# Kernel optimization log

Hardware: AMD Instinct MI355X
Metric: run time of the kernel (lower is better)

## Reference

```python
import jax, jax.numpy as jnp
import numpy as np

S = 3136        # tokens (56x56 patch grid, single image segment -> full attention)
H = 16          # num_heads
D = 80          # head_dim (= head_dim_ori = PADDING_HEAD_DIM)
HID = H * D     # 1280
SCALE = 1.0 / float(np.sqrt(D))  # qkScale = 1/sqrt(head_dim_ori)


def _rope_tables(s, d, base=10000.0):
    # rotate_half style: cos/sin of shape [s, d], duplicated over the two halves
    half = d // 2
    inv_freq = 1.0 / (base ** (np.arange(0, half, dtype=np.float32) / half))
    freqs = np.outer(np.arange(s, dtype=np.float32), inv_freq)  # [s, d/2]
    emb = np.concatenate([freqs, freqs], axis=-1)               # [s, d]
    return jnp.asarray(np.cos(emb)), jnp.asarray(np.sin(emb))


def setup_inputs() -> dict:
    key = jax.random.key(0)
    ks = jax.random.split(key, 6)
    cos, sin = _rope_tables(S, D)
    return {
        "hidden_states": jax.random.normal(ks[0], (S, HID), jnp.float32),
        "x_norm": jax.random.normal(ks[1], (S, HID), jnp.float32),
        "qkv_w": jax.random.normal(ks[2], (3 * HID, HID), jnp.float32) * 0.02,
        "qkv_b": jax.random.normal(ks[3], (3 * HID,), jnp.float32) * 0.02,
        "proj_w": jax.random.normal(ks[4], (HID, HID), jnp.float32) * 0.02,
        "proj_b": jax.random.normal(ks[5], (HID,), jnp.float32) * 0.02,
        "cos": cos,
        "sin": sin,
    }


def _rotate_half(x):
    x1, x2 = jnp.split(x, 2, axis=-1)
    return jnp.concatenate([-x2, x1], axis=-1)


def reference(hidden_states, x_norm, qkv_w, qkv_b, proj_w, proj_b, cos, sin):
    # fused QKV linear (transposeB=True) + split into q,k,v along last dim
    qkv = x_norm @ qkv_w.T + qkv_b                      # [S, 3*HID]
    q, k, v = jnp.split(qkv, 3, axis=-1)                # each [S, HID]
    q = q.reshape(S, H, D)
    k = k.reshape(S, H, D)
    v = v.reshape(S, H, D)
    # inline RoPE on q and k (rotate_half over full head_dim)
    c = cos[:, None, :]; s = sin[:, None, :]           # [S,1,D]
    q = q * c + _rotate_half(q) * s
    k = k * c + _rotate_half(k) * s
    # full self-attention (PA_ENCODER, single segment = seq_len S)
    scores = jnp.einsum('shd,thd->hst', q, k) * SCALE   # [H,S,S]
    probs = jax.nn.softmax(scores, axis=-1)
    attn = jnp.einsum('hst,thd->shd', probs, v)         # [S,H,D]
    attn = attn.reshape(S, HID)
    # output projection + residual add
    out = attn @ proj_w.T + proj_b
    return hidden_states + out
```

## Files before the change

kernel.cpp:

```cpp
#include <hip/hip_runtime.h>
#include <hip/hip_bf16.h>

#define S_   3136
#define H_   16
#define D_   80
#define DP_  96
#define HID_ 1280

typedef short  bf16x8 __attribute__((ext_vector_type(8)));
typedef short  bf16x4 __attribute__((ext_vector_type(4)));
typedef float  f32x4  __attribute__((ext_vector_type(4)));

__device__ __forceinline__ float b2f(unsigned short u) {
    union { unsigned int i; float f; } c;
    c.i = ((unsigned int)u) << 16;
    return c.f;
}
__device__ __forceinline__ unsigned short f2b(float f) {
    union { unsigned int i; float f; } c;
    c.f = f;
    unsigned int x = c.i;
    unsigned int lsb = (x >> 16) & 1u;
    x += 0x7fffu + lsb;
    return (unsigned short)(x >> 16);
}

#define N4_X 1003520
#define N4_Q 1228800
#define N4_P 409600

__global__ __launch_bounds__(256)
void cast3_kernel(const float* __restrict__ x0, unsigned short* __restrict__ y0,
                  const float* __restrict__ x1, unsigned short* __restrict__ y1,
                  const float* __restrict__ x2, unsigned short* __restrict__ y2)
{
    int i = blockIdx.x * 256 + threadIdx.x;
    const float* src; unsigned short* dst;
    if (i < N4_X)               { src = x0; dst = y0; }
    else if (i < N4_X + N4_Q)   { src = x1; dst = y1; i -= N4_X; }
    else if (i < N4_X + N4_Q + N4_P) { src = x2; dst = y2; i -= N4_X + N4_Q; }
    else return;
    float4 v = ((const float4*)src)[i];
    ushort4 o;
    o.x = f2b(v.x); o.y = f2b(v.y); o.z = f2b(v.z); o.w = f2b(v.w);
    ((ushort4*)dst)[i] = o;
}

#define ASTR 40

__global__ __launch_bounds__(256)
void qkv_mfma_kernel(const unsigned short* __restrict__ Ab,
                     const unsigned short* __restrict__ Wb,
                     const float* __restrict__ bias,
                     unsigned short* __restrict__ qo, unsigned short* __restrict__ ko,
                     unsigned short* __restrict__ vtb)
{
    __shared__ __align__(16) short As[128][ASTR];
    __shared__ __align__(16) short Bs[128][ASTR];
    int m0 = blockIdx.x * 128;
    int n0 = blockIdx.y * 128;
    int t = threadIdx.x;
    int wave = t >> 6, lane = t & 63, lq = lane & 15, quad = lane >> 4;
    int wr = wave >> 1, wc = wave & 1;

    int r0  = t >> 2;
    int r1  = r0 + 64;
    int kc0 = (t & 3) << 3;
    const unsigned short* pa0 = Ab + (size_t)min(m0 + r0, S_ - 1) * HID_ + kc0;
    const unsigned short* pa1 = Ab + (size_t)min(m0 + r1, S_ - 1) * HID_ + kc0;
    const unsigned short* pb0 = Wb + (size_t)(n0 + r0) * HID_ + kc0;
    const unsigned short* pb1 = Wb + (size_t)(n0 + r1) * HID_ + kc0;
    short* sa0 = &As[r0][kc0];
    short* sa1 = &As[r1][kc0];
    short* sb0 = &Bs[r0][kc0];
    short* sb1 = &Bs[r1][kc0];

    const bf16x8* afp[4]; const bf16x8* bfp[4];
    #pragma unroll
    for (int i = 0; i < 4; ++i) {
        afp[i] = (const bf16x8*)&As[wr * 64 + i * 16 + lq][quad * 8];
        bfp[i] = (const bf16x8*)&Bs[wc * 64 + i * 16 + lq][quad * 8];
    }

    f32x4 acc[4][4];
    #pragma unroll
    for (int i = 0; i < 4; ++i)
        #pragma unroll
        for (int j = 0; j < 4; ++j) acc[i][j] = (f32x4){0.f, 0.f, 0.f, 0.f};

    bf16x8 va0 = *(const bf16x8*)(pa0);
    bf16x8 va1 = *(const bf16x8*)(pa1);
    bf16x8 vb0 = *(const bf16x8*)(pb0);
    bf16x8 vb1 = *(const bf16x8*)(pb1);

    for (int kt = 0; kt < HID_; kt += 32) {
        __syncthreads();
        *(bf16x8*)sa0 = va0; *(bf16x8*)sa1 = va1;
        *(bf16x8*)sb0 = vb0; *(bf16x8*)sb1 = vb1;
        __syncthreads();
        if (kt + 32 < HID_) {
            va0 = *(const bf16x8*)(pa0 + kt + 32);
            va1 = *(const bf16x8*)(pa1 + kt + 32);
            vb0 = *(const bf16x8*)(pb0 + kt + 32);
            vb1 = *(const bf16x8*)(pb1 + kt + 32);
        }
        bf16x8 af[4], bfr[4];
        #pragma unroll
        for (int i = 0; i < 4; ++i) af[i]  = *afp[i];
        #pragma unroll
        for (int j = 0; j < 4; ++j) bfr[j] = *bfp[j];
        #pragma unroll
        for (int i = 0; i < 4; ++i)
            #pragma unroll
            for (int j = 0; j < 4; ++j)
                acc[i][j] = __builtin_amdgcn_mfma_f32_16x16x32_bf16(af[i], bfr[j], acc[i][j], 0, 0, 0);
    }

    #pragma unroll
    for (int i = 0; i < 4; ++i)
        #pragma unroll
        for (int j = 0; j < 4; ++j)
            #pragma unroll
            for (int reg = 0; reg < 4; ++reg) {
                int row = m0 + wr * 64 + i * 16 + quad * 4 + reg;
                if (row >= S_) continue;
                int col = n0 + wc * 64 + j * 16 + lq;
                float val = acc[i][j][reg] + bias[col];
                int which = col / HID_;
                int rem   = col - which * HID_;
                int h     = rem / D_;
                int d     = rem - h * D_;
                if (which == 0)      qo[((size_t)h * S_ + row) * D_ + d] = f2b(val);
                else if (which == 1) ko[((size_t)h * S_ + row) * D_ + d] = f2b(val);
                else                 vtb[((size_t)h * D_ + d) * S_ + row] = f2b(val);
            }
}

__global__ __launch_bounds__(256)
void proj_mfma_kernel(const unsigned short* __restrict__ Ab,
                      const unsigned short* __restrict__ Wb,
                      const float* __restrict__ bias, const float* __restrict__ hidden,
                      float* __restrict__ out)
{
    __shared__ __align__(16) short As[64][ASTR];
    __shared__ __align__(16) short Bs[64][ASTR];
    int m0 = blockIdx.x * 64;
    int n0 = blockIdx.y * 64;
    int t = threadIdx.x;
    int wave = t >> 6, lane = t & 63, lq = lane & 15, quad = lane >> 4;
    int wr = wave >> 1, wc = wave & 1;

    int r  = t >> 2;
    int kc0 = (t & 3) << 3;
    const unsigned short* pa = Ab + (size_t)(m0 + r) * HID_ + kc0;
    const unsigned short* pb = Wb + (size_t)(n0 + r) * HID_ + kc0;
    short* sa = &As[r][kc0];
    short* sb = &Bs[r][kc0];

    const bf16x8* afp[2]; const bf16x8* bfp[2];
    #pragma unroll
    for (int i = 0; i < 2; ++i) {
        afp[i] = (const bf16x8*)&As[wr * 32 + i * 16 + lq][quad * 8];
        bfp[i] = (const bf16x8*)&Bs[wc * 32 + i * 16 + lq][quad * 8];
    }

    f32x4 acc[2][2];
    #pragma unroll
    for (int i = 0; i < 2; ++i)
        #pragma unroll
        for (int j = 0; j < 2; ++j) acc[i][j] = (f32x4){0.f, 0.f, 0.f, 0.f};

    bf16x8 va = *(const bf16x8*)(pa);
    bf16x8 vb = *(const bf16x8*)(pb);

    for (int kt = 0; kt < HID_; kt += 32) {
        __syncthreads();
        *(bf16x8*)sa = va;
        *(bf16x8*)sb = vb;
        __syncthreads();
        if (kt + 32 < HID_) {
            va = *(const bf16x8*)(pa + kt + 32);
            vb = *(const bf16x8*)(pb + kt + 32);
        }
        bf16x8 af[2], bfr[2];
        #pragma unroll
        for (int i = 0; i < 2; ++i) af[i]  = *afp[i];
        #pragma unroll
        for (int j = 0; j < 2; ++j) bfr[j] = *bfp[j];
        #pragma unroll
        for (int i = 0; i < 2; ++i)
            #pragma unroll
            for (int j = 0; j < 2; ++j)
                acc[i][j] = __builtin_amdgcn_mfma_f32_16x16x32_bf16(af[i], bfr[j], acc[i][j], 0, 0, 0);
    }

    #pragma unroll
    for (int i = 0; i < 2; ++i)
        #pragma unroll
        for (int j = 0; j < 2; ++j)
            #pragma unroll
            for (int reg = 0; reg < 4; ++reg) {
                int row = m0 + wr * 32 + i * 16 + quad * 4 + reg;
                int col = n0 + wc * 32 + j * 16 + lq;
                out[(size_t)row * HID_ + col] =
                    acc[i][j][reg] + bias[col] + hidden[(size_t)row * HID_ + col];
            }
}

__global__ void rope_kernel(const unsigned short* __restrict__ q, const unsigned short* __restrict__ k,
                            const float* __restrict__ cost, const float* __restrict__ sint,
                            unsigned short* __restrict__ qb, unsigned short* __restrict__ kb)
{
    const float QSCALE = 0.11180339887498949f * 1.4426950408889634f;
    int idx = blockIdx.x * 256 + threadIdx.x;
    const int total = H_ * S_ * 40;
    if (idx >= total) return;
    int d  = idx % 40;
    int hs = idx / 40;
    int s  = hs % S_;
    size_t base  = (size_t)hs * D_;
    size_t base9 = (size_t)hs * DP_;
    float c1 = cost[s * D_ + d];
    float s1 = sint[s * D_ + d];
    float c2 = cost[s * D_ + d + 40];
    float s2 = sint[s * D_ + d + 40];
    float x1 = b2f(q[base + d]), x2 = b2f(q[base + d + 40]);
    qb[base9 + d]      = f2b((x1 * c1 - x2 * s1) * QSCALE);
    qb[base9 + d + 40] = f2b((x2 * c2 + x1 * s2) * QSCALE);
    x1 = b2f(k[base + d]); x2 = b2f(k[base + d + 40]);
    kb[base9 + d]      = f2b(x1 * c1 - x2 * s1);
    kb[base9 + d + 40] = f2b(x2 * c2 + x1 * s2);
    if (d < 16) {
        qb[base9 + 80 + d] = 0;
        kb[base9 + 80 + d] = 0;
    }
}

#define KSTRIDE 104
#define VSTRIDE 72
#define PSTRIDE 68

__global__ __launch_bounds__(256)
void attn_kernel(const unsigned short* __restrict__ Qb,
                 const unsigned short* __restrict__ Kb,
                 const unsigned short* __restrict__ Vtb,
                 unsigned short* __restrict__ attnb)
{
    __shared__ __align__(16) short Ks[64][KSTRIDE];
    __shared__ __align__(16) short Vs[2][96][VSTRIDE];
    __shared__ __align__(16) short Ps[4][16][PSTRIDE];

    int h   = blockIdx.y;
    int qb0 = blockIdx.x * 64;
    int t    = threadIdx.x;
    int wave = t >> 6;
    int lane = t & 63;
    int lq   = lane & 15;
    int quad = lane >> 4;

    const unsigned short* Qrow = Qb + ((size_t)h * S_ + qb0 + wave * 16 + lq) * DP_;
    bf16x8 qf[3];
    #pragma unroll
    for (int kc = 0; kc < 3; ++kc)
        qf[kc] = *(const bf16x8*)(Qrow + kc * 32 + quad * 8);

    f32x4 O[5];
    #pragma unroll
    for (int dt = 0; dt < 5; ++dt) O[dt] = (f32x4){0.f, 0.f, 0.f, 0.f};
    float l_acc[4] = {0.f, 0.f, 0.f, 0.f};

    int srow = t & 63;
    int w    = t >> 6;
    int vr0  = t >> 3;
    int vc   = (t & 7) << 3;
    const unsigned short* Kg = Kb  + (size_t)h * S_ * DP_ + (size_t)srow * DP_;
    const unsigned short* Vg = Vtb + (size_t)h * D_ * S_;
    short* kl0 = &Ks[srow][(w    ) * 8];
    short* kl1 = &Ks[srow][(w + 4) * 8];
    short* kl2 = &Ks[srow][(w + 8) * 8];

    const int NKB = S_ / 64;
    bf16x8 pk0, pk1, pk2, pv0, pv1, pv2;
    {
        pk0 = *(const bf16x8*)(Kg + (w    ) * 8);
        pk1 = *(const bf16x8*)(Kg + (w + 4) * 8);
        pk2 = *(const bf16x8*)(Kg + (w + 8) * 8);
        const unsigned short* vg = Vg + vc;
        pv0 = *(const bf16x8*)(vg + (size_t)(vr0     ) * S_);
        pv1 = *(const bf16x8*)(vg + (size_t)(vr0 + 32) * S_);
        pv2 = *(const bf16x8*)(vg + (size_t)(vr0 + 64) * S_);
    }

    for (int kb = 0; kb < NKB; ++kb) {
        int vb = kb & 1;
        __syncthreads();
        *(bf16x8*)kl0 = pk0;
        *(bf16x8*)kl1 = pk1;
        *(bf16x8*)kl2 = pk2;
        *(bf16x8*)&Vs[vb][vr0     ][vc] = pv0;
        *(bf16x8*)&Vs[vb][vr0 + 32][vc] = pv1;
        *(bf16x8*)&Vs[vb][vr0 + 64][vc] = pv2;
        __syncthreads();

        if (kb + 1 < NKB) {
            const unsigned short* kg = Kg + (size_t)(kb + 1) * 64 * DP_;
            pk0 = *(const bf16x8*)(kg + (w    ) * 8);
            pk1 = *(const bf16x8*)(kg + (w + 4) * 8);
            pk2 = *(const bf16x8*)(kg + (w + 8) * 8);
            const unsigned short* vg = Vg + (kb + 1) * 64 + vc;
            pv0 = *(const bf16x8*)(vg + (size_t)(vr0     ) * S_);
            pv1 = *(const bf16x8*)(vg + (size_t)(vr0 + 32) * S_);
            pv2 = *(const bf16x8*)(vg + (size_t)(vr0 + 64) * S_);
        }

        f32x4 sc[4];
        #pragma unroll
        for (int nt = 0; nt < 4; ++nt) {
            sc[nt] = (f32x4){0.f, 0.f, 0.f, 0.f};
            #pragma unroll
            for (int kc = 0; kc < 3; ++kc) {
                bf16x8 kf = *(const bf16x8*)&Ks[nt * 16 + lq][kc * 32 + quad * 8];
                sc[nt] = __builtin_amdgcn_mfma_f32_16x16x32_bf16(qf[kc], kf, sc[nt], 0, 0, 0);
            }
        }

        if (kb > 0) {
            const short (*Vp)[VSTRIDE] = Vs[vb ^ 1];
            #pragma unroll
            for (int kc = 0; kc < 2; ++kc) {
                union { bf16x8 v8; bf16x4 v4[2]; } pf;
                pf.v4[0] = *(const bf16x4*)&Ps[wave][lq][kc * 32 + quad * 8];
                pf.v4[1] = *(const bf16x4*)&Ps[wave][lq][kc * 32 + quad * 8 + 4];
                #pragma unroll
                for (int dt = 0; dt < 5; ++dt) {
                    bf16x8 vf = *(const bf16x8*)&Vp[dt * 16 + lq][kc * 32 + quad * 8];
                    O[dt] = __builtin_amdgcn_mfma_f32_16x16x32_bf16(pf.v8, vf, O[dt], 0, 0, 0);
                }
            }
        }

        #pragma unroll
        for (int reg = 0; reg < 4; ++reg) {
            float p0 = exp2f(sc[0][reg]);
            float p1 = exp2f(sc[1][reg]);
            float p2 = exp2f(sc[2][reg]);
            float p3 = exp2f(sc[3][reg]);
            l_acc[reg] += (p0 + p1) + (p2 + p3);
            int prow = quad * 4 + reg;
            Ps[wave][prow][ 0 + lq] = (short)(__float_as_uint(p0) >> 16);
            Ps[wave][prow][16 + lq] = (short)(__float_as_uint(p1) >> 16);
            Ps[wave][prow][32 + lq] = (short)(__float_as_uint(p2) >> 16);
            Ps[wave][prow][48 + lq] = (short)(__float_as_uint(p3) >> 16);
        }
    }

    {
        const short (*Vp)[VSTRIDE] = Vs[(NKB - 1) & 1];
        #pragma unroll
        for (int kc = 0; kc < 2; ++kc) {
            union { bf16x8 v8; bf16x4 v4[2]; } pf;
            pf.v4[0] = *(const bf16x4*)&Ps[wave][lq][kc * 32 + quad * 8];
            pf.v4[1] = *(const bf16x4*)&Ps[wave][lq][kc * 32 + quad * 8 + 4];
            #pragma unroll
            for (int dt = 0; dt < 5; ++dt) {
                bf16x8 vf = *(const bf16x8*)&Vp[dt * 16 + lq][kc * 32 + quad * 8];
                O[dt] = __builtin_amdgcn_mfma_f32_16x16x32_bf16(pf.v8, vf, O[dt], 0, 0, 0);
            }
        }
    }

    #pragma unroll
    for (int reg = 0; reg < 4; ++reg) {
        float l = l_acc[reg];
        #pragma unroll
        for (int off = 1; off < 16; off <<= 1)
            l += __shfl_xor(l, off, 16);
        float linv = 1.0f / l;
        int s = qb0 + wave * 16 + quad * 4 + reg;
        unsigned short* orow = attnb + (size_t)s * HID_ + h * D_;
        #pragma unroll
        for (int dt = 0; dt < 5; ++dt)
            orow[dt * 16 + lq] = f2b(O[dt][reg] * linv);
    }
}

extern "C" void kernel_launch(void* const* d_in, const int* in_sizes, int n_in,
                              void* d_out, int out_size, void* d_ws, size_t ws_size,
                              hipStream_t stream)
{
    const float* hidden = (const float*)d_in[0];
    const float* x_norm = (const float*)d_in[1];
    const float* qkv_w  = (const float*)d_in[2];
    const float* qkv_b  = (const float*)d_in[3];
    const float* proj_w = (const float*)d_in[4];
    const float* proj_b = (const float*)d_in[5];
    const float* cost   = (const float*)d_in[6];
    const float* sint   = (const float*)d_in[7];
    float* out = (float*)d_out;

    unsigned short* w      = (unsigned short*)d_ws;
    unsigned short* qbuf   = w;
    unsigned short* kbuf   = qbuf + 4014080;
    unsigned short* vtb    = kbuf + 4014080;
    unsigned short* kbb    = vtb + 4064256;
    unsigned short* xb     = kbb + 4816896;
    unsigned short* wqkvb  = xb + 4014080;
    unsigned short* wprojb = wqkvb + 4915200;
    unsigned short* qbb    = wqkvb;
    unsigned short* abuf   = qbuf;

    cast3_kernel<<<(N4_X + N4_Q + N4_P + 255) / 256, 256, 0, stream>>>(
        x_norm, xb, qkv_w, wqkvb, proj_w, wprojb);

    qkv_mfma_kernel<<<dim3(25, 30), 256, 0, stream>>>(xb, wqkvb, qkv_b, qbuf, kbuf, vtb);
    rope_kernel<<<(H_ * S_ * 40 + 255) / 256, 256, 0, stream>>>(qbuf, kbuf, cost, sint, qbb, kbb);
    attn_kernel<<<dim3(S_ / 64, H_), 256, 0, stream>>>(qbb, kbb, vtb, abuf);
    proj_mfma_kernel<<<dim3(49, 20), 256, 0, stream>>>(abuf, wprojb, proj_b, hidden, out);
}
```

Before: 372.9 us.

## Double K-step per sync in QKV GEMM and drop skewed PV pipeline in attention

The QKV GEMM now stages two 32-wide K slices per iteration into two shared buffers, halving the number of barrier pairs and issuing twice as many global loads in flight per step, at the cost of more LDS and registers. The attention kernel drops the software-skewed PV step that used a double-buffered V tile and the previous block's probabilities. It now does the PV MFMA right after writing P within the same iteration, using a single V buffer. That lowers LDS use and may raise occupancy, but QK and PV are no longer interleaved across iterations to hide latency.

```diff
diff --git a/kernel.cpp b/kernel.cpp
--- a/kernel.cpp
+++ b/kernel.cpp
@@ -55,8 +55,8 @@
                      unsigned short* __restrict__ qo, unsigned short* __restrict__ ko,
                      unsigned short* __restrict__ vtb)
 {
-    __shared__ __align__(16) short As[128][ASTR];
-    __shared__ __align__(16) short Bs[128][ASTR];
+    __shared__ __align__(16) short As[2][128][ASTR];
+    __shared__ __align__(16) short Bs[2][128][ASTR];
     int m0 = blockIdx.x * 128;
     int n0 = blockIdx.y * 128;
     int t = threadIdx.x;
@@ -70,17 +70,15 @@
     const unsigned short* pa1 = Ab + (size_t)min(m0 + r1, S_ - 1) * HID_ + kc0;
     const unsigned short* pb0 = Wb + (size_t)(n0 + r0) * HID_ + kc0;
     const unsigned short* pb1 = Wb + (size_t)(n0 + r1) * HID_ + kc0;
-    short* sa0 = &As[r0][kc0];
-    short* sa1 = &As[r1][kc0];
-    short* sb0 = &Bs[r0][kc0];
-    short* sb1 = &Bs[r1][kc0];
-
-    const bf16x8* afp[4]; const bf16x8* bfp[4];
-    #pragma unroll
-    for (int i = 0; i < 4; ++i) {
-        afp[i] = (const bf16x8*)&As[wr * 64 + i * 16 + lq][quad * 8];
-        bfp[i] = (const bf16x8*)&Bs[wc * 64 + i * 16 + lq][quad * 8];
-    }
+
+    const bf16x8* afp[2][4]; const bf16x8* bfp[2][4];
+    #pragma unroll
+    for (int s = 0; s < 2; ++s)
+        #pragma unroll
+        for (int i = 0; i < 4; ++i) {
+            afp[s][i] = (const bf16x8*)&As[s][wr * 64 + i * 16 + lq][quad * 8];
+            bfp[s][i] = (const bf16x8*)&Bs[s][wc * 64 + i * 16 + lq][quad * 8];
+        }
 
     f32x4 acc[4][4];
     #pragma unroll
@@ -88,32 +86,47 @@
         #pragma unroll
         for (int j = 0; j < 4; ++j) acc[i][j] = (f32x4){0.f, 0.f, 0.f, 0.f};
 
-    bf16x8 va0 = *(const bf16x8*)(pa0);
-    bf16x8 va1 = *(const bf16x8*)(pa1);
-    bf16x8 vb0 = *(const bf16x8*)(pb0);
-    bf16x8 vb1 = *(const bf16x8*)(pb1);
-
-    for (int kt = 0; kt < HID_; kt += 32) {
-        __syncthreads();
-        *(bf16x8*)sa0 = va0; *(bf16x8*)sa1 = va1;
-        *(bf16x8*)sb0 = vb0; *(bf16x8*)sb1 = vb1;
-        __syncthreads();
-        if (kt + 32 < HID_) {
-            va0 = *(const bf16x8*)(pa0 + kt + 32);
-            va1 = *(const bf16x8*)(pa1 + kt + 32);
-            vb0 = *(const bf16x8*)(pb0 + kt + 32);
-            vb1 = *(const bf16x8*)(pb1 + kt + 32);
-        }
-        bf16x8 af[4], bfr[4];
-        #pragma unroll
-        for (int i = 0; i < 4; ++i) af[i]  = *afp[i];
-        #pragma unroll
-        for (int j = 0; j < 4; ++j) bfr[j] = *bfp[j];
-        #pragma unroll
-        for (int i = 0; i < 4; ++i)
-            #pragma unroll
-            for (int j = 0; j < 4; ++j)
-                acc[i][j] = __builtin_amdgcn_mfma_f32_16x16x32_bf16(af[i], bfr[j], acc[i][j], 0, 0, 0);
+    bf16x8 va[2][2], vb[2][2];
+    #pragma unroll
+    for (int s = 0; s < 2; ++s) {
+        va[s][0] = *(const bf16x8*)(pa0 + s * 32);
+        va[s][1] = *(const bf16x8*)(pa1 + s * 32);
+        vb[s][0] = *(const bf16x8*)(pb0 + s * 32);
+        vb[s][1] = *(const bf16x8*)(pb1 + s * 32);
+    }
+
+    for (int kt = 0; kt < HID_; kt += 64) {
+        __syncthreads();
+        #pragma unroll
+        for (int s = 0; s < 2; ++s) {
+            *(bf16x8*)&As[s][r0][kc0] = va[s][0];
+            *(bf16x8*)&As[s][r1][kc0] = va[s][1];
+            *(bf16x8*)&Bs[s][r0][kc0] = vb[s][0];
+            *(bf16x8*)&Bs[s][r1][kc0] = vb[s][1];
+        }
+        __syncthreads();
+        if (kt + 64 < HID_) {
+            #pragma unroll
+            for (int s = 0; s < 2; ++s) {
+                va[s][0] = *(const bf16x8*)(pa0 + kt + 64 + s * 32);
+                va[s][1] = *(const bf16x8*)(pa1 + kt + 64 + s * 32);
+                vb[s][0] = *(const bf16x8*)(pb0 + kt + 64 + s * 32);
+                vb[s][1] = *(const bf16x8*)(pb1 + kt + 64 + s * 32);
+            }
+        }
+        #pragma unroll
+        for (int s = 0; s < 2; ++s) {
+            bf16x8 af[4], bfr[4];
+            #pragma unroll
+            for (int i = 0; i < 4; ++i) af[i]  = *afp[s][i];
+            #pragma unroll
+            for (int j = 0; j < 4; ++j) bfr[j] = *bfp[s][j];
+            #pragma unroll
+            for (int i = 0; i < 4; ++i)
+                #pragma unroll
+                for (int j = 0; j < 4; ++j)
+                    acc[i][j] = __builtin_amdgcn_mfma_f32_16x16x32_bf16(af[i], bfr[j], acc[i][j], 0, 0, 0);
+        }
     }
 
     #pragma unroll
@@ -247,7 +260,7 @@
                  unsigned short* __restrict__ attnb)
 {
     __shared__ __align__(16) short Ks[64][KSTRIDE];
-    __shared__ __align__(16) short Vs[2][96][VSTRIDE];
+    __shared__ __align__(16) short Vs[96][VSTRIDE];
     __shared__ __align__(16) short Ps[4][16][PSTRIDE];
 
     int h   = blockIdx.y;
@@ -292,14 +305,13 @@
     }
 
     for (int kb = 0; kb < NKB; ++kb) {
-        int vb = kb & 1;
         __syncthreads();
         *(bf16x8*)kl0 = pk0;
         *(bf16x8*)kl1 = pk1;
         *(bf16x8*)kl2 = pk2;
-        *(bf16x8*)&Vs[vb][vr0     ][vc] = pv0;
-        *(bf16x8*)&Vs[vb][vr0 + 32][vc] = pv1;
-        *(bf16x8*)&Vs[vb][vr0 + 64][vc] = pv2;
+        *(bf16x8*)&Vs[vr0     ][vc] = pv0;
+        *(bf16x8*)&Vs[vr0 + 32][vc] = pv1;
+        *(bf16x8*)&Vs[vr0 + 64][vc] = pv2;
         __syncthreads();
 
         if (kb + 1 < NKB) {
@@ -321,21 +333,6 @@
             for (int kc = 0; kc < 3; ++kc) {
                 bf16x8 kf = *(const bf16x8*)&Ks[nt * 16 + lq][kc * 32 + quad * 8];
                 sc[nt] = __builtin_amdgcn_mfma_f32_16x16x32_bf16(qf[kc], kf, sc[nt], 0, 0, 0);
-            }
-        }
-
-        if (kb > 0) {
-            const short (*Vp)[VSTRIDE] = Vs[vb ^ 1];
-            #pragma unroll
-            for (int kc = 0; kc < 2; ++kc) {
-                union { bf16x8 v8; bf16x4 v4[2]; } pf;
-                pf.v4[0] = *(const bf16x4*)&Ps[wave][lq][kc * 32 + quad * 8];
-                pf.v4[1] = *(const bf16x4*)&Ps[wave][lq][kc * 32 + quad * 8 + 4];
-                #pragma unroll
-                for (int dt = 0; dt < 5; ++dt) {
-                    bf16x8 vf = *(const bf16x8*)&Vp[dt * 16 + lq][kc * 32 + quad * 8];
-                    O[dt] = __builtin_amdgcn_mfma_f32_16x16x32_bf16(pf.v8, vf, O[dt], 0, 0, 0);
-                }
             }
         }
 
@@ -352,10 +349,7 @@
             Ps[wave][prow][32 + lq] = (short)(__float_as_uint(p2) >> 16);
             Ps[wave][prow][48 + lq] = (short)(__float_as_uint(p3) >> 16);
         }
-    }
-
-    {
-        const short (*Vp)[VSTRIDE] = Vs[(NKB - 1) & 1];
+
         #pragma unroll
         for (int kc = 0; kc < 2; ++kc) {
             union { bf16x8 v8; bf16x4 v4[2]; } pf;
@@ -363,7 +357,7 @@
             pf.v4[1] = *(const bf16x4*)&Ps[wave][lq][kc * 32 + quad * 8 + 4];
             #pragma unroll
             for (int dt = 0; dt < 5; ++dt) {
-                bf16x8 vf = *(const bf16x8*)&Vp[dt * 16 + lq][kc * 32 + quad * 8];
+                bf16x8 vf = *(const bf16x8*)&Vs[dt * 16 + lq][kc * 32 + quad * 8];
                 O[dt] = __builtin_amdgcn_mfma_f32_16x16x32_bf16(pf.v8, vf, O[dt], 0, 0, 0);
             }
         }
```

Result: faster. 343.9 us (-7.8%).
